# Kernel optimization log

Measured on AMD Instinct MI355X. Metric: run time of the kernel, lower is better.

Reference implementation:

```python
import jax, jax.numpy as jnp
import numpy as np

O, T, DIN, H, DOUT = 50000, 500000, 128, 256, 128


def setup_inputs() -> dict:
    key = jax.random.key(0)
    ks = jax.random.split(key, 12)
    s = 0.05
    return {
        "obj_vecs": jax.random.normal(ks[0], (O, DIN), jnp.float32),
        "pred_vecs": jax.random.normal(ks[1], (T, DIN), jnp.float32),
        "edges": jax.random.randint(ks[2], (T, 2), 0, O, jnp.int64),
        "w1a": jax.random.normal(ks[3], (3 * DIN, H), jnp.float32) * s,
        "b1a": jax.random.normal(ks[4], (H,), jnp.float32) * s,
        "w1b": jax.random.normal(ks[5], (H, 2 * H + DOUT), jnp.float32) * s,
        "b1b": jax.random.normal(ks[6], (2 * H + DOUT,), jnp.float32) * s,
        "w2a": jax.random.normal(ks[7], (H, H), jnp.float32) * s,
        "b2a": jax.random.normal(ks[8], (H,), jnp.float32) * s,
        "w2b": jax.random.normal(ks[9], (H, DOUT), jnp.float32) * s,
        "b2b": jax.random.normal(ks[10], (DOUT,), jnp.float32) * s,
    }


def reference(obj_vecs, pred_vecs, edges, w1a, b1a, w1b, b1b, w2a, b2a, w2b, b2b):
    n_obj = obj_vecs.shape[0]
    h_dim = w2a.shape[0]
    d_out = w2b.shape[1]
    s_idx = edges[:, 0]
    o_idx = edges[:, 1]
    # gather subject/object node features, concat with predicate: [T, 3*Din]
    cur_t = jnp.concatenate([obj_vecs[s_idx], pred_vecs, obj_vecs[o_idx]], axis=1)
    # edge MLP (net1): Linear-ReLU-Linear-ReLU -> [T, 2H + Dout]
    new_t = jax.nn.relu(jax.nn.relu(cur_t @ w1a + b1a) @ w1b + b1b)
    new_s = new_t[:, :h_dim]
    new_p = new_t[:, h_dim:h_dim + d_out]
    new_o = new_t[:, h_dim + d_out:]
    # scatter-add pooling back to nodes, both endpoints
    idx = jnp.concatenate([s_idx, o_idx])
    vals = jnp.concatenate([new_s, new_o], axis=0)
    pooled = jax.ops.segment_sum(vals, idx, num_segments=n_obj)
    # avg pooling: divide by per-node incidence count (clamped to >= 1)
    counts = jax.ops.segment_sum(jnp.ones(idx.shape[0], obj_vecs.dtype), idx,
                                 num_segments=n_obj)
    pooled = pooled / jnp.clip(counts, 1.0)[:, None]
    # node MLP (net2)
    new_obj = jax.nn.relu(jax.nn.relu(pooled @ w2a + b2a) @ w2b + b2b)
    return new_obj, new_p
```

## Files before the change

kernel.cpp:

```cpp
#include <hip/hip_runtime.h>


using f32x4 = __attribute__((ext_vector_type(4))) float;
using s16x8 = __attribute__((ext_vector_type(8))) short;
typedef unsigned short u16x8 __attribute__((ext_vector_type(8)));

static __device__ __forceinline__ unsigned short f2b(float f) {
    unsigned int u = __float_as_uint(f);
    unsigned int r = (u + 0x7fffu + ((u >> 16) & 1u)) >> 16;
    return (unsigned short)r;
}

static __device__ __forceinline__ float b2f(unsigned short b) {
    return __uint_as_float(((unsigned)b) << 16);
}

static __device__ __forceinline__ unsigned swz(unsigned row, unsigned byteoff) {
    return byteoff ^ ((row & 7u) << 4);
}

static __device__ __forceinline__ void gload_lds16(const unsigned short* g, unsigned short* l) {
    __builtin_amdgcn_global_load_lds(
        (const __attribute__((address_space(1))) unsigned int*)g,
        (__attribute__((address_space(3))) unsigned int*)l,
        16, 0, 0);
}

__global__ void prep_weights(const float* __restrict__ w1a, const float* __restrict__ w1b,
                             const float* __restrict__ w2a, const float* __restrict__ w2b,
                             unsigned short* __restrict__ w1aT, unsigned short* __restrict__ w1bT,
                             unsigned short* __restrict__ w2aT, unsigned short* __restrict__ w2bT) {
    int t = blockIdx.x * blockDim.x + threadIdx.x;
    if (t < 2 * 6 * 8192) {
        int tile = t >> 13; int nc1 = tile / 6, kt = tile % 6;
        int rem = t & 8191; int c = rem >> 6, kk = rem & 63;
        unsigned byte = ((unsigned)(c * 128 + kk * 2)) ^ ((c & 7u) << 4);
        *(unsigned short*)((char*)w1aT + (size_t)tile * 16384 + byte) =
            f2b(w1a[(size_t)(kt * 64 + kk) * 256 + nc1 * 128 + c]);
        return;
    }
    t -= 98304;
    if (t < 5 * 4 * 8192) {
        int tile = t >> 13; int nc = tile >> 2, kt2 = tile & 3;
        int rem = t & 8191; int c = rem >> 6, kk = rem & 63;
        unsigned byte = ((unsigned)(c * 128 + kk * 2)) ^ ((c & 7u) << 4);
        *(unsigned short*)((char*)w1bT + (size_t)tile * 16384 + byte) =
            f2b(w1b[(size_t)(kt2 * 64 + kk) * 640 + nc * 128 + c]);
        return;
    }
    t -= 163840;
    if (t < 65536) { int n = t >> 8, k = t & 255; w2aT[t] = f2b(w2a[k * 256 + n]); return; }
    t -= 65536;
    if (t < 32768) { int n = t >> 8, k = t & 255; w2bT[t] = f2b(w2b[k * 128 + n]); return; }
}

__global__ void count_kernel_i(const int* __restrict__ edges, int* __restrict__ cnt, int T) {
    int e = blockIdx.x * blockDim.x + threadIdx.x;
    if (e < T) {
        atomicAdd(&cnt[edges[2 * (long long)e]], 1);
        atomicAdd(&cnt[edges[2 * (long long)e + 1]], 1);
    }
}

__global__ void scan_kernel(const int* __restrict__ cnt, int* __restrict__ rowptr,
                            int* __restrict__ cursor, int O) {
    __shared__ int sc[1024];
    const int tid = threadIdx.x;
    const int per = (O + 1023) >> 10;
    const int base = tid * per;
    int s = 0;
    for (int i = 0; i < per; ++i) { int j = base + i; if (j < O) s += cnt[j]; }
    sc[tid] = s;
    __syncthreads();
    for (int d = 1; d < 1024; d <<= 1) {
        int v = (tid >= d) ? sc[tid - d] : 0;
        __syncthreads();
        sc[tid] += v;
        __syncthreads();
    }
    int off = sc[tid] - s;
    for (int i = 0; i < per; ++i) {
        int j = base + i;
        if (j < O) { rowptr[j] = off; cursor[j] = off; off += cnt[j]; }
    }
    if (tid == 0) rowptr[O] = sc[1023];
}

__global__ void fill_kernel(const int* __restrict__ edges, int* __restrict__ cursor,
                            int* __restrict__ csr, int T) {
    int e = blockIdx.x * blockDim.x + threadIdx.x;
    if (e < T) {
        int s = edges[2 * (long long)e];
        int o = edges[2 * (long long)e + 1];
        int ps = atomicAdd(&cursor[s], 1); csr[ps] = e;
        int po = atomicAdd(&cursor[o], 1); csr[po] = T + e;
    }
}

__global__ __launch_bounds__(256, 2) void edge_mlp(
    const float* __restrict__ obj, const float* __restrict__ pred,
    const int* __restrict__ edges,
    const unsigned short* __restrict__ w1aT, const float* __restrict__ b1a,
    const unsigned short* __restrict__ w1bT, const float* __restrict__ b1b,
    unsigned short* __restrict__ edgeout, float* __restrict__ outP, int T) {
    const int m0 = blockIdx.x * 64;
    const int tid = threadIdx.x;
    const int lane = tid & 63, wid = tid >> 6;
    const int wm = wid >> 1, wn = wid & 1;
    const bool evenL = ((lane & 1) == 0);

    __shared__ unsigned short U[32768];
    char* const ldsb = (char*)U;
    unsigned short* const abuf0 = (unsigned short*)(ldsb);
    unsigned short* const abuf1 = (unsigned short*)(ldsb + 8192);
    unsigned short* const Hbuf  = (unsigned short*)(ldsb);
    unsigned short* const bbuf0 = (unsigned short*)(ldsb + 32768);
    unsigned short* const bbuf1 = (unsigned short*)(ldsb + 49152);

    bool okR[2][4];
    #pragma unroll
    for (int mi = 0; mi < 2; ++mi)
        #pragma unroll
        for (int rr = 0; rr < 4; ++rr)
            okR[mi][rr] = (m0 + wm * 32 + mi * 16 + ((lane >> 4) << 2) + rr) < T;

    const int r = tid >> 2;
    const int q = tid & 3;
    int e_r = m0 + r; if (e_r >= T) e_r = T - 1;
    const int sIdx_r = edges[2 * (long long)e_r];
    const int oIdx_r = edges[2 * (long long)e_r + 1];

    auto aSrc = [&](int kt) -> const float4* {
        const float* s;
        if (kt < 2)      s = obj  + (long long)sIdx_r * 128 + kt * 64;
        else if (kt < 4) s = pred + (long long)e_r   * 128 + (kt - 2) * 64;
        else             s = obj  + (long long)oIdx_r * 128 + (kt - 4) * 64;
        return (const float4*)s;
    };

    auto stageB = [&](const unsigned short* gt, unsigned short* bb) {
        #pragma unroll
        for (int rr4 = 0; rr4 < 4; ++rr4) {
            unsigned off = wid * 4096u + rr4 * 1024u;
            gload_lds16((const unsigned short*)((const char*)gt + off + lane * 16u),
                        (unsigned short*)((char*)bb + off));
        }
    };

    auto writeA = [&](const float4* ap, unsigned short* ab) {
        #pragma unroll
        for (int i = 0; i < 4; ++i) {
            float4 v = ap[i];
            ushort4 pk; pk.x = f2b(v.x); pk.y = f2b(v.y); pk.z = f2b(v.z); pk.w = f2b(v.w);
            unsigned byte = (r * 128u + q * 32u + i * 8u) ^ ((r & 7u) << 4);
            *(ushort4*)((char*)ab + byte) = pk;
        }
    };

    f32x4 acc1[2][2][4];
    #pragma unroll
    for (int a = 0; a < 2; ++a)
        #pragma unroll
        for (int b = 0; b < 2; ++b)
            #pragma unroll
            for (int c = 0; c < 4; ++c) acc1[a][b][c] = f32x4{0.f, 0.f, 0.f, 0.f};

    auto mfma1 = [&](const unsigned short* ab, const unsigned short* bb, int nc1) {
        #pragma unroll
        for (int ks = 0; ks < 2; ++ks) {
            const unsigned kk = ks * 32u + ((lane >> 4) << 3);
            s16x8 af[2];
            #pragma unroll
            for (int mi = 0; mi < 2; ++mi) {
                unsigned row = wm * 32u + mi * 16u + (lane & 15);
                af[mi] = *(const s16x8*)((const char*)ab + ((row * 128u + kk * 2u) ^ ((row & 7u) << 4)));
            }
            #pragma unroll
            for (int nj = 0; nj < 4; ++nj) {
                unsigned c = wn * 64u + nj * 16u + (lane & 15);
                s16x8 bf = *(const s16x8*)((const char*)bb + ((c * 128u + kk * 2u) ^ ((c & 7u) << 4)));
                #pragma unroll
                for (int mi = 0; mi < 2; ++mi)
                    acc1[nc1][mi][nj] = __builtin_amdgcn_mfma_f32_16x16x32_bf16(af[mi], bf, acc1[nc1][mi][nj], 0, 0, 0);
            }
        }
    };

    float4 ap[4];
    {
        const float4* s4 = aSrc(0);
        #pragma unroll
        for (int i = 0; i < 4; ++i) ap[i] = s4[q * 4 + i];
    }
    stageB(w1aT + (size_t)(0 * 6 + 0) * 8192, bbuf0);
    writeA(ap, abuf0);
    __syncthreads();

    #pragma unroll
    for (int kt = 0; kt < 6; ++kt) {
        unsigned short* const ab = (kt & 1) ? abuf1 : abuf0;
        stageB(w1aT + (size_t)(1 * 6 + kt) * 8192, bbuf1);
        if (kt < 5) {
            const float4* s4 = aSrc(kt + 1);
            #pragma unroll
            for (int i = 0; i < 4; ++i) ap[i] = s4[q * 4 + i];
        }
        mfma1(ab, bbuf0, 0);
        __syncthreads();
        if (kt < 5) stageB(w1aT + (size_t)(0 * 6 + (kt + 1)) * 8192, bbuf0);
        mfma1(ab, bbuf1, 1);
        if (kt < 5) writeA(ap, (kt & 1) ? abuf0 : abuf1);
        __syncthreads();
    }

    stageB(w1bT, bbuf0);
    #pragma unroll
    for (int nb = 0; nb < 2; ++nb)
        #pragma unroll
        for (int nj = 0; nj < 4; ++nj) {
            int col = nb * 128 + wn * 64 + nj * 16 + (lane & 15);
            float bias = b1a[col];
            #pragma unroll
            for (int mi = 0; mi < 2; ++mi)
                #pragma unroll
                for (int rr = 0; rr < 4; ++rr) {
                    unsigned row = wm * 32u + mi * 16u + ((lane >> 4) << 2) + rr;
                    float v = acc1[nb][mi][nj][rr] + bias;
                    v = v > 0.f ? v : 0.f;
                    *(unsigned short*)((char*)Hbuf + swz(row, row * 512u + col * 2u)) = f2b(v);
                }
        }
    __syncthreads();

    #pragma unroll
    for (int nc = 0; nc < 5; ++nc) {
        f32x4 acc2[2][4];
        #pragma unroll
        for (int b = 0; b < 2; ++b)
            #pragma unroll
            for (int c = 0; c < 4; ++c) acc2[b][c] = f32x4{0.f, 0.f, 0.f, 0.f};

        #pragma unroll
        for (int kt2 = 0; kt2 < 4; ++kt2) {
            if (kt2 < 3)           stageB(w1bT + (size_t)(nc * 4 + kt2 + 1) * 8192, (kt2 & 1) ? bbuf0 : bbuf1);
            else if (nc < 4)       stageB(w1bT + (size_t)((nc + 1) * 4) * 8192, bbuf0);
            unsigned short* const bb = (kt2 & 1) ? bbuf1 : bbuf0;
            #pragma unroll
            for (int ks = 0; ks < 2; ++ks) {
                const unsigned kkB = ks * 32u + ((lane >> 4) << 3);
                const unsigned kkH = kt2 * 64u + kkB;
                s16x8 af[2];
                #pragma unroll
                for (int mi = 0; mi < 2; ++mi) {
                    unsigned row = wm * 32u + mi * 16u + (lane & 15);
                    af[mi] = *(const s16x8*)((const char*)Hbuf + swz(row, row * 512u + kkH * 2u));
                }
                #pragma unroll
                for (int nj = 0; nj < 4; ++nj) {
                    unsigned c = wn * 64u + nj * 16u + (lane & 15);
                    s16x8 bf = *(const s16x8*)((const char*)bb + ((c * 128u + kkB * 2u) ^ ((c & 7u) << 4)));
                    #pragma unroll
                    for (int mi = 0; mi < 2; ++mi)
                        acc2[mi][nj] = __builtin_amdgcn_mfma_f32_16x16x32_bf16(af[mi], bf, acc2[mi][nj], 0, 0, 0);
                }
            }
            __syncthreads();
        }

        if (nc == 2) {
            #pragma unroll
            for (int nj = 0; nj < 4; ++nj) {
                int col = nc * 128 + wn * 64 + nj * 16 + (lane & 15);
                float bias = b1b[col];
                #pragma unroll
                for (int mi = 0; mi < 2; ++mi)
                    #pragma unroll
                    for (int rr = 0; rr < 4; ++rr) {
                        int row = wm * 32 + mi * 16 + ((lane >> 4) << 2) + rr;
                        if (okR[mi][rr]) {
                            float v = acc2[mi][nj][rr] + bias;
                            v = v > 0.f ? v : 0.f;
                            outP[(long long)(m0 + row) * 128 + (col - 256)] = v;
                        }
                    }
            }
        } else {
            #pragma unroll
            for (int nj = 0; nj < 4; ++nj) {
                int col = nc * 128 + wn * 64 + nj * 16 + (lane & 15);
                float bias = b1b[col];
                int pc = (nc < 2) ? col : (col - 384);
                int pcb = (lane & 1) ? (pc - 1) : pc;
                #pragma unroll
                for (int mi = 0; mi < 2; ++mi) {
                    float vv[4];
                    #pragma unroll
                    for (int rr = 0; rr < 4; ++rr) {
                        float v = acc2[mi][nj][rr] + bias;
                        vv[rr] = v > 0.f ? v : 0.f;
                    }
                    float nb0 = __shfl_xor(vv[0], 1);
                    float nb1 = __shfl_xor(vv[1], 1);
                    float nb2 = __shfl_xor(vv[2], 1);
                    float nb3 = __shfl_xor(vv[3], 1);
                    #pragma unroll
                    for (int k = 0; k < 2; ++k) {
                        float lo = evenL ? (k ? vv[1] : vv[0]) : (k ? nb3 : nb2);
                        float hi = evenL ? (k ? nb1 : nb0) : (k ? vv[3] : vv[2]);
                        int rsel = evenL ? k : 2 + k;
                        if (okR[mi][rsel]) {
                            int row = wm * 32 + mi * 16 + ((lane >> 4) << 2) + rsel;
                            size_t e = (size_t)(m0 + row);
                            size_t rid = (nc < 2) ? e : (size_t)T + e;
                            unsigned pk = ((unsigned)f2b(hi) << 16) | f2b(lo);
                            *(unsigned*)(edgeout + rid * 256 + pcb) = pk;
                        }
                    }
                }
            }
        }
    }
}

__global__ __launch_bounds__(256, 4) void pool_gather(
    const unsigned short* __restrict__ edgeout, const int* __restrict__ rowptr,
    const int* __restrict__ csr, unsigned short* __restrict__ pooled, int O) {
    int w = blockIdx.x * 4 + (threadIdx.x >> 6);
    if (w >= O) return;
    const int lane = threadIdx.x & 63;
    const int beg = rowptr[w], end = rowptr[w + 1];
    float ax = 0.f, ay = 0.f, az = 0.f, aw = 0.f;
    float bx = 0.f, by = 0.f, bz = 0.f, bw = 0.f;
    int i = beg;
    for (; i + 1 < end; i += 2) {
        int r0 = csr[i], r1 = csr[i + 1];
        ushort4 v0 = *(const ushort4*)(edgeout + (size_t)r0 * 256 + lane * 4);
        ushort4 v1 = *(const ushort4*)(edgeout + (size_t)r1 * 256 + lane * 4);
        ax += b2f(v0.x); ay += b2f(v0.y); az += b2f(v0.z); aw += b2f(v0.w);
        bx += b2f(v1.x); by += b2f(v1.y); bz += b2f(v1.z); bw += b2f(v1.w);
    }
    if (i < end) {
        int r0 = csr[i];
        ushort4 v0 = *(const ushort4*)(edgeout + (size_t)r0 * 256 + lane * 4);
        ax += b2f(v0.x); ay += b2f(v0.y); az += b2f(v0.z); aw += b2f(v0.w);
    }
    float inv = 1.f / fmaxf((float)(end - beg), 1.f);
    ushort4 o4;
    o4.x = f2b((ax + bx) * inv); o4.y = f2b((ay + by) * inv);
    o4.z = f2b((az + bz) * inv); o4.w = f2b((aw + bw) * inv);
    *(ushort4*)(pooled + (size_t)w * 256 + lane * 4) = o4;
}

__global__ __launch_bounds__(256, 2) void obj_mlp(
    const unsigned short* __restrict__ pooled,
    const unsigned short* __restrict__ w2aT, const float* __restrict__ b2a,
    const unsigned short* __restrict__ w2bT, const float* __restrict__ b2b,
    float* __restrict__ outObj, int O) {
    const int m0 = blockIdx.x * 64;
    const int tid = threadIdx.x;
    const int lane = tid & 63, wid = tid >> 6;
    const int wm = wid >> 1, wn = wid & 1;

    __shared__ unsigned short Abuf[64 * 256];

    {
        const int r = tid >> 2, q = tid & 3;
        int objc = m0 + r; if (objc >= O) objc = O - 1;
        const u16x8* s8 = (const u16x8*)(pooled + (size_t)objc * 256);
        #pragma unroll
        for (int i = 0; i < 8; ++i) {
            u16x8 v = s8[q * 8 + i];
            unsigned byte = r * 512u + (q * 64u + i * 8u) * 2u;
            *(u16x8*)((char*)Abuf + swz(r, byte)) = v;
        }
    }
    __syncthreads();

    f32x4 acc1[2][2][4];
    #pragma unroll
    for (int a = 0; a < 2; ++a)
        #pragma unroll
        for (int b = 0; b < 2; ++b)
            #pragma unroll
            for (int c = 0; c < 4; ++c) acc1[a][b][c] = f32x4{0.f, 0.f, 0.f, 0.f};
    #pragma unroll
    for (int ks = 0; ks < 8; ++ks) {
        const int klane = ks * 32 + ((lane >> 4) << 3);
        s16x8 af[2];
        #pragma unroll
        for (int mi = 0; mi < 2; ++mi) {
            int row = wm * 32 + mi * 16 + (lane & 15);
            af[mi] = *(const s16x8*)((const char*)Abuf + swz(row, row * 512u + klane * 2u));
        }
        #pragma unroll
        for (int nb = 0; nb < 2; ++nb)
            #pragma unroll
            for (int nj = 0; nj < 4; ++nj) {
                int col = nb * 128 + wn * 64 + nj * 16 + (lane & 15);
                s16x8 bf = *(const s16x8*)(w2aT + (long long)col * 256 + klane);
                #pragma unroll
                for (int mi = 0; mi < 2; ++mi)
                    acc1[nb][mi][nj] = __builtin_amdgcn_mfma_f32_16x16x32_bf16(af[mi], bf, acc1[nb][mi][nj], 0, 0, 0);
            }
    }
    __syncthreads();

    #pragma unroll
    for (int nb = 0; nb < 2; ++nb)
        #pragma unroll
        for (int nj = 0; nj < 4; ++nj) {
            int col = nb * 128 + wn * 64 + nj * 16 + (lane & 15);
            float bias = b2a[col];
            #pragma unroll
            for (int mi = 0; mi < 2; ++mi)
                #pragma unroll
                for (int rr = 0; rr < 4; ++rr) {
                    int row = wm * 32 + mi * 16 + ((lane >> 4) << 2) + rr;
                    float v = acc1[nb][mi][nj][rr] + bias;
                    v = v > 0.f ? v : 0.f;
                    *(unsigned short*)((char*)Abuf + swz(row, row * 512u + col * 2u)) = f2b(v);
                }
        }
    __syncthreads();

    f32x4 acc2[2][4];
    #pragma unroll
    for (int b = 0; b < 2; ++b)
        #pragma unroll
        for (int c = 0; c < 4; ++c) acc2[b][c] = f32x4{0.f, 0.f, 0.f, 0.f};
    #pragma unroll
    for (int ks = 0; ks < 8; ++ks) {
        const int klane = ks * 32 + ((lane >> 4) << 3);
        s16x8 af[2];
        #pragma unroll
        for (int mi = 0; mi < 2; ++mi) {
            int row = wm * 32 + mi * 16 + (lane & 15);
            af[mi] = *(const s16x8*)((const char*)Abuf + swz(row, row * 512u + klane * 2u));
        }
        #pragma unroll
        for (int nj = 0; nj < 4; ++nj) {
            int col = wn * 64 + nj * 16 + (lane & 15);
            s16x8 bf = *(const s16x8*)(w2bT + (long long)col * 256 + klane);
            #pragma unroll
            for (int mi = 0; mi < 2; ++mi)
                acc2[mi][nj] = __builtin_amdgcn_mfma_f32_16x16x32_bf16(af[mi], bf, acc2[mi][nj], 0, 0, 0);
        }
    }

    #pragma unroll
    for (int nj = 0; nj < 4; ++nj) {
        int col = wn * 64 + nj * 16 + (lane & 15);
        float bias = b2b[col];
        #pragma unroll
        for (int mi = 0; mi < 2; ++mi)
            #pragma unroll
            for (int rr = 0; rr < 4; ++rr) {
                int row = wm * 32 + mi * 16 + ((lane >> 4) << 2) + rr;
                int o = m0 + row;
                if (o < O) {
                    float v = acc2[mi][nj][rr] + bias;
                    v = v > 0.f ? v : 0.f;
                    outObj[(long long)o * 128 + col] = v;
                }
            }
    }
}

extern "C" void kernel_launch(void* const* d_in, const int* in_sizes, int n_in,
                              void* d_out, int out_size, void* d_ws, size_t ws_size,
                              hipStream_t stream) {
    const float* obj  = (const float*)d_in[0];
    const float* pred = (const float*)d_in[1];
    const int*   edges = (const int*)d_in[2];
    const float* w1a = (const float*)d_in[3];
    const float* b1a = (const float*)d_in[4];
    const float* w1b = (const float*)d_in[5];
    const float* b1b = (const float*)d_in[6];
    const float* w2a = (const float*)d_in[7];
    const float* b2a = (const float*)d_in[8];
    const float* w2b = (const float*)d_in[9];
    const float* b2b = (const float*)d_in[10];

    const int O = in_sizes[0] / 128;
    const int T = in_sizes[1] / 128;

    auto al = [](size_t x) { return (x + 255) & ~(size_t)255; };
    const size_t szEdgeout = (size_t)2 * T * 256 * 2;
    const size_t szPooled  = (size_t)O * 256 * 2;
    const size_t szCnt     = (size_t)O * 4;
    const size_t szRow     = (size_t)(O + 1) * 4;
    const size_t szCsr     = (size_t)2 * T * 4;

    size_t off = 0;
    char* ws = (char*)d_ws;
    unsigned short* edgeout = (unsigned short*)(ws + off); off += al(szEdgeout);
    unsigned short* pooled  = (unsigned short*)(ws + off); off += al(szPooled);
    int* cnt    = (int*)(ws + off); off += al(szCnt);
    int* cursor = (int*)(ws + off); off += al(szCnt);
    int* rowptr = (int*)(ws + off); off += al(szRow);
    int* csr    = (int*)(ws + off); off += al(szCsr);
    unsigned short* w1aT = (unsigned short*)(ws + off); off += (size_t)12 * 8192 * 2;
    unsigned short* w1bT = (unsigned short*)(ws + off); off += (size_t)20 * 8192 * 2;
    unsigned short* w2aT = (unsigned short*)(ws + off); off += (size_t)256 * 256 * 2;
    unsigned short* w2bT = (unsigned short*)(ws + off);

    float* outObj = (float*)d_out;
    float* outP   = (float*)d_out + (size_t)O * 128;

    hipMemsetAsync(cnt, 0, szCnt, stream);
    const int prepElems = 98304 + 163840 + 65536 + 32768;
    prep_weights<<<(prepElems + 255) / 256, 256, 0, stream>>>(w1a, w1b, w2a, w2b, w1aT, w1bT, w2aT, w2bT);
    count_kernel_i<<<(T + 255) / 256, 256, 0, stream>>>(edges, cnt, T);
    scan_kernel<<<1, 1024, 0, stream>>>(cnt, rowptr, cursor, O);
    fill_kernel<<<(T + 255) / 256, 256, 0, stream>>>(edges, cursor, csr, T);
    edge_mlp<<<(T + 63) / 64, 256, 0, stream>>>(obj, pred, edges, w1aT, b1a, w1bT, b1b, edgeout, outP, T);
    pool_gather<<<(O + 3) / 4, 256, 0, stream>>>(edgeout, rowptr, csr, pooled, O);
    obj_mlp<<<(O + 63) / 64, 256, 0, stream>>>(pooled, w2aT, b2a, w2bT, b2b, outObj, O);
}
```

Measured before the change: 1.017 ms.

## Enlarge edge MLP tile to 128 rows with 8 waves and wider weight tiles

The edge MLP block now covers 128 edges with 512 threads (8 waves) instead of 64 edges with 256 threads. Weight tiles are re-laid out so the first layer stages all 256 output columns per k-step and the second layer uses 128-deep k tiles. The main loops are restructured to match, with one sync per step. The aim is more reuse of each staged weight tile across rows and fewer barriers and staging steps per edge. In exchange, LDS per block doubles to 128 KB, which may cap occupancy, and register pressure per wave goes up.

```diff
diff --git a/kernel.cpp b/kernel.cpp
--- a/kernel.cpp
+++ b/kernel.cpp
@@ -31,21 +31,21 @@
                              unsigned short* __restrict__ w1aT, unsigned short* __restrict__ w1bT,
                              unsigned short* __restrict__ w2aT, unsigned short* __restrict__ w2bT) {
     int t = blockIdx.x * blockDim.x + threadIdx.x;
-    if (t < 2 * 6 * 8192) {
-        int tile = t >> 13; int nc1 = tile / 6, kt = tile % 6;
-        int rem = t & 8191; int c = rem >> 6, kk = rem & 63;
+    if (t < 6 * 16384) {
+        int kt = t >> 14;
+        int rem = t & 16383; int c = rem >> 6, kk = rem & 63;
         unsigned byte = ((unsigned)(c * 128 + kk * 2)) ^ ((c & 7u) << 4);
-        *(unsigned short*)((char*)w1aT + (size_t)tile * 16384 + byte) =
-            f2b(w1a[(size_t)(kt * 64 + kk) * 256 + nc1 * 128 + c]);
+        *(unsigned short*)((char*)w1aT + (size_t)kt * 32768 + byte) =
+            f2b(w1a[(size_t)(kt * 64 + kk) * 256 + c]);
         return;
     }
     t -= 98304;
-    if (t < 5 * 4 * 8192) {
-        int tile = t >> 13; int nc = tile >> 2, kt2 = tile & 3;
-        int rem = t & 8191; int c = rem >> 6, kk = rem & 63;
-        unsigned byte = ((unsigned)(c * 128 + kk * 2)) ^ ((c & 7u) << 4);
-        *(unsigned short*)((char*)w1bT + (size_t)tile * 16384 + byte) =
-            f2b(w1b[(size_t)(kt2 * 64 + kk) * 640 + nc * 128 + c]);
+    if (t < 10 * 16384) {
+        int tile = t >> 14; int nc = tile >> 1, kh = tile & 1;
+        int rem = t & 16383; int c = rem >> 7, kk = rem & 127;
+        unsigned byte = ((unsigned)(c * 256 + kk * 2)) ^ ((c & 7u) << 4);
+        *(unsigned short*)((char*)w1bT + (size_t)tile * 32768 + byte) =
+            f2b(w1b[(size_t)(kh * 128 + kk) * 640 + nc * 128 + c]);
         return;
     }
     t -= 163840;
@@ -97,32 +97,32 @@
     }
 }
 
-__global__ __launch_bounds__(256, 2) void edge_mlp(
+__global__ __launch_bounds__(512, 2) void edge_mlp(
     const float* __restrict__ obj, const float* __restrict__ pred,
     const int* __restrict__ edges,
     const unsigned short* __restrict__ w1aT, const float* __restrict__ b1a,
     const unsigned short* __restrict__ w1bT, const float* __restrict__ b1b,
     unsigned short* __restrict__ edgeout, float* __restrict__ outP, int T) {
-    const int m0 = blockIdx.x * 64;
+    const int m0 = blockIdx.x * 128;
     const int tid = threadIdx.x;
     const int lane = tid & 63, wid = tid >> 6;
-    const int wm = wid >> 1, wn = wid & 1;
+    const int wm = wid >> 2, wn = wid & 3;
     const bool evenL = ((lane & 1) == 0);
 
-    __shared__ unsigned short U[32768];
+    __shared__ unsigned short U[65536];
     char* const ldsb = (char*)U;
     unsigned short* const abuf0 = (unsigned short*)(ldsb);
-    unsigned short* const abuf1 = (unsigned short*)(ldsb + 8192);
+    unsigned short* const abuf1 = (unsigned short*)(ldsb + 16384);
     unsigned short* const Hbuf  = (unsigned short*)(ldsb);
-    unsigned short* const bbuf0 = (unsigned short*)(ldsb + 32768);
-    unsigned short* const bbuf1 = (unsigned short*)(ldsb + 49152);
-
-    bool okR[2][4];
-    #pragma unroll
-    for (int mi = 0; mi < 2; ++mi)
+    unsigned short* const bbuf0 = (unsigned short*)(ldsb + 65536);
+    unsigned short* const bbuf1 = (unsigned short*)(ldsb + 98304);
+
+    bool okR[4][4];
+    #pragma unroll
+    for (int mi = 0; mi < 4; ++mi)
         #pragma unroll
         for (int rr = 0; rr < 4; ++rr)
-            okR[mi][rr] = (m0 + wm * 32 + mi * 16 + ((lane >> 4) << 2) + rr) < T;
+            okR[mi][rr] = (m0 + wm * 64 + mi * 16 + ((lane >> 4) << 2) + rr) < T;
 
     const int r = tid >> 2;
     const int q = tid & 3;
@@ -157,22 +157,20 @@
         }
     };
 
-    f32x4 acc1[2][2][4];
-    #pragma unroll
-    for (int a = 0; a < 2; ++a)
-        #pragma unroll
-        for (int b = 0; b < 2; ++b)
-            #pragma unroll
-            for (int c = 0; c < 4; ++c) acc1[a][b][c] = f32x4{0.f, 0.f, 0.f, 0.f};
-
-    auto mfma1 = [&](const unsigned short* ab, const unsigned short* bb, int nc1) {
+    f32x4 acc1[4][4];
+    #pragma unroll
+    for (int a = 0; a < 4; ++a)
+        #pragma unroll
+        for (int b = 0; b < 4; ++b) acc1[a][b] = f32x4{0.f, 0.f, 0.f, 0.f};
+
+    auto mfma1 = [&](const unsigned short* ab, const unsigned short* bb) {
         #pragma unroll
         for (int ks = 0; ks < 2; ++ks) {
             const unsigned kk = ks * 32u + ((lane >> 4) << 3);
-            s16x8 af[2];
-            #pragma unroll
-            for (int mi = 0; mi < 2; ++mi) {
-                unsigned row = wm * 32u + mi * 16u + (lane & 15);
+            s16x8 af[4];
+            #pragma unroll
+            for (int mi = 0; mi < 4; ++mi) {
+                unsigned row = wm * 64u + mi * 16u + (lane & 15);
                 af[mi] = *(const s16x8*)((const char*)ab + ((row * 128u + kk * 2u) ^ ((row & 7u) << 4)));
             }
             #pragma unroll
@@ -180,8 +178,8 @@
                 unsigned c = wn * 64u + nj * 16u + (lane & 15);
                 s16x8 bf = *(const s16x8*)((const char*)bb + ((c * 128u + kk * 2u) ^ ((c & 7u) << 4)));
                 #pragma unroll
-                for (int mi = 0; mi < 2; ++mi)
-                    acc1[nc1][mi][nj] = __builtin_amdgcn_mfma_f32_16x16x32_bf16(af[mi], bf, acc1[nc1][mi][nj], 0, 0, 0);
+                for (int mi = 0; mi < 4; ++mi)
+                    acc1[mi][nj] = __builtin_amdgcn_mfma_f32_16x16x32_bf16(af[mi], bf, acc1[mi][nj], 0, 0, 0);
             }
         }
     };
@@ -192,75 +190,69 @@
         #pragma unroll
         for (int i = 0; i < 4; ++i) ap[i] = s4[q * 4 + i];
     }
-    stageB(w1aT + (size_t)(0 * 6 + 0) * 8192, bbuf0);
+    stageB(w1aT, bbuf0);
     writeA(ap, abuf0);
     __syncthreads();
 
     #pragma unroll
     for (int kt = 0; kt < 6; ++kt) {
-        unsigned short* const ab = (kt & 1) ? abuf1 : abuf0;
-        stageB(w1aT + (size_t)(1 * 6 + kt) * 8192, bbuf1);
         if (kt < 5) {
             const float4* s4 = aSrc(kt + 1);
             #pragma unroll
             for (int i = 0; i < 4; ++i) ap[i] = s4[q * 4 + i];
-        }
-        mfma1(ab, bbuf0, 0);
+            stageB(w1aT + (size_t)(kt + 1) * 16384, ((kt + 1) & 1) ? bbuf1 : bbuf0);
+        }
+        mfma1((kt & 1) ? abuf1 : abuf0, (kt & 1) ? bbuf1 : bbuf0);
+        if (kt < 5) writeA(ap, ((kt + 1) & 1) ? abuf1 : abuf0);
         __syncthreads();
-        if (kt < 5) stageB(w1aT + (size_t)(0 * 6 + (kt + 1)) * 8192, bbuf0);
-        mfma1(ab, bbuf1, 1);
-        if (kt < 5) writeA(ap, (kt & 1) ? abuf0 : abuf1);
-        __syncthreads();
     }
 
     stageB(w1bT, bbuf0);
     #pragma unroll
-    for (int nb = 0; nb < 2; ++nb)
-        #pragma unroll
-        for (int nj = 0; nj < 4; ++nj) {
-            int col = nb * 128 + wn * 64 + nj * 16 + (lane & 15);
-            float bias = b1a[col];
-            #pragma unroll
-            for (int mi = 0; mi < 2; ++mi)
-                #pragma unroll
-                for (int rr = 0; rr < 4; ++rr) {
-                    unsigned row = wm * 32u + mi * 16u + ((lane >> 4) << 2) + rr;
-                    float v = acc1[nb][mi][nj][rr] + bias;
-                    v = v > 0.f ? v : 0.f;
-                    *(unsigned short*)((char*)Hbuf + swz(row, row * 512u + col * 2u)) = f2b(v);
-                }
-        }
+    for (int nj = 0; nj < 4; ++nj) {
+        int col = wn * 64 + nj * 16 + (lane & 15);
+        float bias = b1a[col];
+        #pragma unroll
+        for (int mi = 0; mi < 4; ++mi)
+            #pragma unroll
+            for (int rr = 0; rr < 4; ++rr) {
+                unsigned row = wm * 64u + mi * 16u + ((lane >> 4) << 2) + rr;
+                float v = acc1[mi][nj][rr] + bias;
+                v = v > 0.f ? v : 0.f;
+                *(unsigned short*)((char*)Hbuf + swz(row, row * 512u + col * 2u)) = f2b(v);
+            }
+    }
     __syncthreads();
 
     #pragma unroll
     for (int nc = 0; nc < 5; ++nc) {
-        f32x4 acc2[2][4];
-        #pragma unroll
-        for (int b = 0; b < 2; ++b)
-            #pragma unroll
-            for (int c = 0; c < 4; ++c) acc2[b][c] = f32x4{0.f, 0.f, 0.f, 0.f};
-
-        #pragma unroll
-        for (int kt2 = 0; kt2 < 4; ++kt2) {
-            if (kt2 < 3)           stageB(w1bT + (size_t)(nc * 4 + kt2 + 1) * 8192, (kt2 & 1) ? bbuf0 : bbuf1);
-            else if (nc < 4)       stageB(w1bT + (size_t)((nc + 1) * 4) * 8192, bbuf0);
-            unsigned short* const bb = (kt2 & 1) ? bbuf1 : bbuf0;
-            #pragma unroll
-            for (int ks = 0; ks < 2; ++ks) {
+        f32x4 acc2[4][2];
+        #pragma unroll
+        for (int a = 0; a < 4; ++a)
+            #pragma unroll
+            for (int b = 0; b < 2; ++b) acc2[a][b] = f32x4{0.f, 0.f, 0.f, 0.f};
+
+        #pragma unroll
+        for (int kh = 0; kh < 2; ++kh) {
+            const int t10 = nc * 2 + kh;
+            if (t10 < 9) stageB(w1bT + (size_t)(t10 + 1) * 16384, ((t10 + 1) & 1) ? bbuf1 : bbuf0);
+            const unsigned short* bb = (t10 & 1) ? bbuf1 : bbuf0;
+            #pragma unroll
+            for (int ks = 0; ks < 4; ++ks) {
                 const unsigned kkB = ks * 32u + ((lane >> 4) << 3);
-                const unsigned kkH = kt2 * 64u + kkB;
-                s16x8 af[2];
-                #pragma unroll
-                for (int mi = 0; mi < 2; ++mi) {
-                    unsigned row = wm * 32u + mi * 16u + (lane & 15);
+                const unsigned kkH = kh * 128u + kkB;
+                s16x8 af[4];
+                #pragma unroll
+                for (int mi = 0; mi < 4; ++mi) {
+                    unsigned row = wm * 64u + mi * 16u + (lane & 15);
                     af[mi] = *(const s16x8*)((const char*)Hbuf + swz(row, row * 512u + kkH * 2u));
                 }
                 #pragma unroll
-                for (int nj = 0; nj < 4; ++nj) {
-                    unsigned c = wn * 64u + nj * 16u + (lane & 15);
-                    s16x8 bf = *(const s16x8*)((const char*)bb + ((c * 128u + kkB * 2u) ^ ((c & 7u) << 4)));
+                for (int nj = 0; nj < 2; ++nj) {
+                    unsigned c = wn * 32u + nj * 16u + (lane & 15);
+                    s16x8 bf = *(const s16x8*)((const char*)bb + ((c * 256u + kkB * 2u) ^ ((c & 7u) << 4)));
                     #pragma unroll
-                    for (int mi = 0; mi < 2; ++mi)
+                    for (int mi = 0; mi < 4; ++mi)
                         acc2[mi][nj] = __builtin_amdgcn_mfma_f32_16x16x32_bf16(af[mi], bf, acc2[mi][nj], 0, 0, 0);
                 }
             }
@@ -269,14 +261,14 @@
 
         if (nc == 2) {
             #pragma unroll
-            for (int nj = 0; nj < 4; ++nj) {
-                int col = nc * 128 + wn * 64 + nj * 16 + (lane & 15);
+            for (int nj = 0; nj < 2; ++nj) {
+                int col = nc * 128 + wn * 32 + nj * 16 + (lane & 15);
                 float bias = b1b[col];
                 #pragma unroll
-                for (int mi = 0; mi < 2; ++mi)
+                for (int mi = 0; mi < 4; ++mi)
                     #pragma unroll
                     for (int rr = 0; rr < 4; ++rr) {
-                        int row = wm * 32 + mi * 16 + ((lane >> 4) << 2) + rr;
+                        int row = wm * 64 + mi * 16 + ((lane >> 4) << 2) + rr;
                         if (okR[mi][rr]) {
                             float v = acc2[mi][nj][rr] + bias;
                             v = v > 0.f ? v : 0.f;
@@ -286,13 +278,13 @@
             }
         } else {
             #pragma unroll
-            for (int nj = 0; nj < 4; ++nj) {
-                int col = nc * 128 + wn * 64 + nj * 16 + (lane & 15);
+            for (int nj = 0; nj < 2; ++nj) {
+                int col = nc * 128 + wn * 32 + nj * 16 + (lane & 15);
                 float bias = b1b[col];
                 int pc = (nc < 2) ? col : (col - 384);
                 int pcb = (lane & 1) ? (pc - 1) : pc;
                 #pragma unroll
-                for (int mi = 0; mi < 2; ++mi) {
+                for (int mi = 0; mi < 4; ++mi) {
                     float vv[4];
                     #pragma unroll
                     for (int rr = 0; rr < 4; ++rr) {
@@ -309,7 +301,7 @@
                         float hi = evenL ? (k ? nb1 : nb0) : (k ? vv[3] : vv[2]);
                         int rsel = evenL ? k : 2 + k;
                         if (okR[mi][rsel]) {
-                            int row = wm * 32 + mi * 16 + ((lane >> 4) << 2) + rsel;
+                            int row = wm * 64 + mi * 16 + ((lane >> 4) << 2) + rsel;
                             size_t e = (size_t)(m0 + row);
                             size_t rid = (nc < 2) ? e : (size_t)T + e;
                             unsigned pk = ((unsigned)f2b(hi) << 16) | f2b(lo);
@@ -499,8 +491,8 @@
     int* cursor = (int*)(ws + off); off += al(szCnt);
     int* rowptr = (int*)(ws + off); off += al(szRow);
     int* csr    = (int*)(ws + off); off += al(szCsr);
-    unsigned short* w1aT = (unsigned short*)(ws + off); off += (size_t)12 * 8192 * 2;
-    unsigned short* w1bT = (unsigned short*)(ws + off); off += (size_t)20 * 8192 * 2;
+    unsigned short* w1aT = (unsigned short*)(ws + off); off += (size_t)6 * 16384 * 2;
+    unsigned short* w1bT = (unsigned short*)(ws + off); off += (size_t)10 * 16384 * 2;
     unsigned short* w2aT = (unsigned short*)(ws + off); off += (size_t)256 * 256 * 2;
     unsigned short* w2bT = (unsigned short*)(ws + off);
 
@@ -513,7 +505,7 @@
     count_kernel_i<<<(T + 255) / 256, 256, 0, stream>>>(edges, cnt, T);
     scan_kernel<<<1, 1024, 0, stream>>>(cnt, rowptr, cursor, O);
     fill_kernel<<<(T + 255) / 256, 256, 0, stream>>>(edges, cursor, csr, T);
-    edge_mlp<<<(T + 63) / 64, 256, 0, stream>>>(obj, pred, edges, w1aT, b1a, w1bT, b1b, edgeout, outP, T);
+    edge_mlp<<<(T + 127) / 128, 512, 0, stream>>>(obj, pred, edges, w1aT, b1a, w1bT, b1b, edgeout, outP, T);
     pool_gather<<<(O + 3) / 4, 256, 0, stream>>>(edgeout, rowptr, csr, pooled, O);
     obj_mlp<<<(O + 63) / 64, 256, 0, stream>>>(pooled, w2aT, b2a, w2bT, b2b, outObj, O);
 }
```

After: 1.003 ms. About the same (-1.4%).
